# Optimization experiments

Hardware: AMD Instinct MI355X
Metric: run time of the kernel (lower is better)

The kernel has to match this reference:

```python
import jax, jax.numpy as jnp
import numpy as np

N_NODES = 100000
N_EDGES = 800000
IN_CH = 100
HID = 100   # 2 * out_channels
OUT = 50


def setup_inputs() -> dict:
    key = jax.random.key(0)
    ks = jax.random.split(key, 6)
    x = jax.random.normal(ks[0], (N_NODES, IN_CH), dtype=jnp.float32)
    edge_index = jax.random.randint(ks[1], (2, N_EDGES), 0, N_NODES, dtype=jnp.int32)
    # Glorot-ish init for the three GCN layer weights; zero biases.
    W1 = jax.random.normal(ks[2], (IN_CH, HID), dtype=jnp.float32) * (1.0 / np.sqrt(IN_CH))
    b1 = jnp.zeros((HID,), dtype=jnp.float32)
    W_mu = jax.random.normal(ks[3], (HID, OUT), dtype=jnp.float32) * (1.0 / np.sqrt(HID))
    b_mu = jnp.zeros((OUT,), dtype=jnp.float32)
    W_ls = jax.random.normal(ks[4], (HID, OUT), dtype=jnp.float32) * (1.0 / np.sqrt(HID))
    b_ls = jnp.zeros((OUT,), dtype=jnp.float32)
    return {"x": x, "edge_index": edge_index, "W1": W1, "b1": b1,
            "W_mu": W_mu, "b_mu": b_mu, "W_ls": W_ls, "b_ls": b_ls}


def _gcn_conv(x, W, b, src, dst, deg_inv_sqrt, n):
    # GCNConv: out = D^-1/2 (A + I) D^-1/2 (x W) + b
    h = x @ W                                      # transform first (smaller messages)
    norm = deg_inv_sqrt[src] * deg_inv_sqrt[dst]   # [E]
    agg = jax.ops.segment_sum(h[src] * norm[:, None], dst, num_segments=n)
    agg = agg + h * (deg_inv_sqrt * deg_inv_sqrt)[:, None]  # self-loop term
    return agg + b


def reference(x, edge_index, W1, b1, W_mu, b_mu, W_ls, b_ls):
    n = x.shape[0]
    src, dst = edge_index[0], edge_index[1]
    # degree with self-loops (GCN normalization, edge_weight = 1)
    deg = jax.ops.segment_sum(jnp.ones((edge_index.shape[1],), jnp.float32), dst,
                              num_segments=n) + 1.0
    deg_inv_sqrt = jax.lax.rsqrt(deg)
    h = jax.nn.relu(_gcn_conv(x, W1, b1, src, dst, deg_inv_sqrt, n))
    # dropout is identity in eval mode (p applied only during training)
    mu = _gcn_conv(h, W_mu, b_mu, src, dst, deg_inv_sqrt, n)
    logstd = _gcn_conv(h, W_ls, b_ls, src, dst, deg_inv_sqrt, n)
    return mu, logstd
```

## Files before the change

kernel.cpp:

```cpp
#include <hip/hip_runtime.h>

#define NN 100000
#define NE 800000
#define NBLK 196
#define BCAP 6144
#define EPB 8192
#define NPART ((NE + EPB - 1) / EPB)
#define PACKBLK 56
#define HS 112

typedef unsigned short ushort_t;
typedef unsigned int uint_t;
typedef __attribute__((ext_vector_type(8))) short short8;
typedef __attribute__((ext_vector_type(4))) float floatx4;

__device__ __forceinline__ float bf2f(ushort_t u) {
    union { unsigned int i; float f; } v; v.i = ((unsigned int)u) << 16; return v.f;
}
__device__ __forceinline__ ushort_t f2bf(float f) {
    union { float f; unsigned int i; } v; v.f = f;
    unsigned int b = v.i + 0x7FFF + ((v.i >> 16) & 1);
    return (ushort_t)(b >> 16);
}
__device__ __forceinline__ uint_t pack2(float a, float b) {
    return (uint_t)f2bf(a) | ((uint_t)f2bf(b) << 16);
}

__global__ __launch_bounds__(256) void k_part(const int* __restrict__ src,
                                              const int* __restrict__ dst,
                                              int* __restrict__ bcnt,
                                              int* __restrict__ bedge,
                                              const float* __restrict__ W1,
                                              const float* __restrict__ Wmu,
                                              const float* __restrict__ Wls,
                                              uint_t* __restrict__ Wt1g,
                                              uint_t* __restrict__ Wt2g) {
    __shared__ int hist[NBLK];
    __shared__ int lbase[NBLK];
    const int blk = blockIdx.x, t = threadIdx.x;

    if (blk >= NPART) {
        int lidx = (blk - NPART) * 256 + t;
        int np = lidx >> 6;
        int kp = lidx & 63;
        int mat = np / 112, n = np - mat * 112;
        int k0 = kp * 2, k1 = k0 + 1;
        float w0 = 0.0f, w1 = 0.0f;
        if (mat == 0) {
            if (n < 100) {
                if (k0 < 100) w0 = W1[k0 * 100 + n];
                if (k1 < 100) w1 = W1[k1 * 100 + n];
            }
            Wt1g[n * 64 + kp] = pack2(w0, w1);
        } else {
            if (n < 50) {
                if (k0 < 100) w0 = Wmu[k0 * 50 + n];
                if (k1 < 100) w1 = Wmu[k1 * 50 + n];
            } else if (n < 100) {
                if (k0 < 100) w0 = Wls[k0 * 50 + (n - 50)];
                if (k1 < 100) w1 = Wls[k1 * 50 + (n - 50)];
            }
            Wt2g[n * 64 + kp] = pack2(w0, w1);
        }
        return;
    }

    const int e0 = blk * EPB;
    const int e1 = (e0 + EPB < NE) ? e0 + EPB : NE;

    if (t < NBLK) hist[t] = 0;
    __syncthreads();
    for (int e = e0 + t; e < e1; e += 256)
        atomicAdd(&hist[dst[e] >> 9], 1);
    __syncthreads();
    if (t < NBLK) {
        int h = hist[t];
        lbase[t] = (h > 0) ? atomicAdd(&bcnt[t], h) : 0;
    }
    __syncthreads();
    if (t < NBLK) hist[t] = lbase[t];
    __syncthreads();
    for (int e = e0 + t; e < e1; e += 256) {
        int d = dst[e];
        int b = d >> 9;
        int pos = atomicAdd(&hist[b], 1);
        bedge[b * BCAP + pos] = src[e] | ((d & 511) << 17);
    }
}

__global__ __launch_bounds__(256) void k_build(const int* __restrict__ bcnt,
                                               const int* __restrict__ bedge,
                                               float* __restrict__ dis,
                                               int* __restrict__ off,
                                               int* __restrict__ ssrc) {
    __shared__ int eb[BCAP];
    __shared__ int hist[512];
    __shared__ int sc[2][512];
    __shared__ int red[4];
    const int b = blockIdx.x, t = threadIdx.x;
    const int cnt = bcnt[b];
    const int* be = bedge + (size_t)b * BCAP;
    const int g0 = b * 512;

    hist[t] = 0; hist[t + 256] = 0;
    int part = (t < b) ? bcnt[t] : 0;
    #pragma unroll
    for (int o = 32; o > 0; o >>= 1) part += __shfl_down(part, o, 64);
    if ((t & 63) == 0) red[t >> 6] = part;
    __syncthreads();

    for (int i = t; i < cnt; i += 256) {
        int v = be[i];
        eb[i] = v;
        atomicAdd(&hist[v >> 17], 1);
    }
    __syncthreads();
    const int base0 = red[0] + red[1] + red[2] + red[3];

    sc[0][t] = hist[t];
    sc[0][t + 256] = hist[t + 256];
    __syncthreads();
    int c = 0;
    for (int o = 1; o < 512; o <<= 1) {
        int nxt = c ^ 1;
        #pragma unroll
        for (int q = 0; q < 2; ++q) {
            int j = t + q * 256;
            sc[nxt][j] = sc[c][j] + ((j >= o) ? sc[c][j - o] : 0);
        }
        c = nxt;
        __syncthreads();
    }

    #pragma unroll
    for (int q = 0; q < 2; ++q) {
        int j = t + q * 256, g = g0 + j;
        int o = base0 + ((j > 0) ? sc[c][j - 1] : 0);
        if (g < NN) dis[g] = rsqrtf((float)hist[j] + 1.0f);
        if (g <= NN) off[g] = o;
        hist[j] = o;
    }
    __syncthreads();

    for (int i = t; i < cnt; i += 256) {
        int v = eb[i];
        int pos = atomicAdd(&hist[v >> 17], 1);
        ssrc[pos] = v & 0x1FFFF;
    }
}

__global__ __launch_bounds__(256) void k_gemm1_mfma(
    const float* __restrict__ X, const uint_t* __restrict__ Wtg,
    const float* __restrict__ dis,
    ushort_t* __restrict__ H)
{
    __shared__ ushort_t Ws[112 * 136];
    const int tid = threadIdx.x;
    const int row0 = blockIdx.x * 64;

    for (int idx = tid; idx < 112 * 16; idx += 256) {
        int n = idx >> 4, c = idx & 15;
        uint4 v = *(const uint4*)&Wtg[n * 64 + c * 4];
        *(uint4*)&Ws[n * 136 + c * 8] = v;
    }
    __syncthreads();

    const int wave = tid >> 6, lane = tid & 63;
    const int quad = lane >> 4, l16 = lane & 15;
    int row = row0 + wave * 16 + l16;
    if (row >= NN) row = NN - 1;
    const float* xp = X + (size_t)row * 100;

    floatx4 acc[7];
    #pragma unroll
    for (int t = 0; t < 7; ++t) acc[t] = (floatx4){0.f, 0.f, 0.f, 0.f};

    #pragma unroll
    for (int ks = 0; ks < 4; ++ks) {
        const int kb = ks * 32 + quad * 8;
        short8 af;
        if (ks < 3) {
            float4 u = *(const float4*)&xp[kb];
            float4 v = *(const float4*)&xp[kb + 4];
            af[0] = (short)f2bf(u.x); af[1] = (short)f2bf(u.y);
            af[2] = (short)f2bf(u.z); af[3] = (short)f2bf(u.w);
            af[4] = (short)f2bf(v.x); af[5] = (short)f2bf(v.y);
            af[6] = (short)f2bf(v.z); af[7] = (short)f2bf(v.w);
        } else {
            af = (short8){0, 0, 0, 0, 0, 0, 0, 0};
            if (quad == 0) {
                float4 u = *(const float4*)&xp[96];
                af[0] = (short)f2bf(u.x); af[1] = (short)f2bf(u.y);
                af[2] = (short)f2bf(u.z); af[3] = (short)f2bf(u.w);
            }
        }
        #pragma unroll
        for (int t = 0; t < 7; ++t) {
            short8 bf = *(const short8*)&Ws[(t * 16 + l16) * 136 + kb];
            acc[t] = __builtin_amdgcn_mfma_f32_16x16x32_bf16(af, bf, acc[t], 0, 0, 0);
        }
    }

    const int mbase = row0 + wave * 16 + quad * 4;
    #pragma unroll
    for (int reg = 0; reg < 4; ++reg) {
        int m = mbase + reg;
        if (m >= NN) continue;
        float dd = dis[m];
        #pragma unroll
        for (int t = 0; t < 7; ++t) {
            int n = t * 16 + l16;
            H[(size_t)m * HS + n] = (n < 100) ? f2bf(acc[t][reg] * dd) : (ushort_t)0;
        }
    }
}

__global__ __launch_bounds__(256) void k_gemm2_mfma(
    const ushort_t* __restrict__ A,
    const uint_t* __restrict__ Wtg,
    const float* __restrict__ bmu, const float* __restrict__ bls,
    float* __restrict__ outmu, float* __restrict__ outls)
{
    __shared__ ushort_t Ws[112 * 136];
    const int tid = threadIdx.x;
    const int row0 = blockIdx.x * 64;

    for (int idx = tid; idx < 112 * 16; idx += 256) {
        int n = idx >> 4, c = idx & 15;
        uint4 v = *(const uint4*)&Wtg[n * 64 + c * 4];
        *(uint4*)&Ws[n * 136 + c * 8] = v;
    }
    __syncthreads();

    const int wave = tid >> 6, lane = tid & 63;
    const int quad = lane >> 4, l16 = lane & 15;
    int arow = row0 + wave * 16 + l16;
    if (arow >= NN) arow = NN - 1;
    const ushort_t* ap = A + (size_t)arow * HS;

    floatx4 acc[7];
    #pragma unroll
    for (int t = 0; t < 7; ++t) acc[t] = (floatx4){0.f, 0.f, 0.f, 0.f};

    #pragma unroll
    for (int ks = 0; ks < 4; ++ks) {
        const int k0 = ks * 32;
        short8 af;
        if (ks < 3) {
            af = *(const short8*)&ap[k0 + quad * 8];
        } else {
            if (quad < 2) af = *(const short8*)&ap[96 + quad * 8];
            else af = (short8){0, 0, 0, 0, 0, 0, 0, 0};
        }
        #pragma unroll
        for (int t = 0; t < 7; ++t) {
            short8 bf = *(const short8*)&Ws[(t * 16 + l16) * 136 + k0 + quad * 8];
            acc[t] = __builtin_amdgcn_mfma_f32_16x16x32_bf16(af, bf, acc[t], 0, 0, 0);
        }
    }

    const int mbase = row0 + wave * 16 + quad * 4;
    #pragma unroll
    for (int reg = 0; reg < 4; ++reg) {
        int m = mbase + reg;
        if (m >= NN) continue;
        #pragma unroll
        for (int t = 0; t < 7; ++t) {
            int n = t * 16 + l16;
            if (n < 50) {
                outmu[(size_t)m * 50 + n] = acc[t][reg] + bmu[n];
            } else if (n < 100) {
                outls[(size_t)m * 50 + (n - 50)] = acc[t][reg] + bls[n - 50];
            }
        }
    }
}

template<int PHASE>
__global__ __launch_bounds__(256, 4) void k_agg(
    const ushort_t* __restrict__ Hin,
    const int* __restrict__ off, const int* __restrict__ ssrc,
    const float* __restrict__ dis, const float* __restrict__ bias,
    ushort_t* __restrict__ outb)
{
    int i = blockIdx.x * 256 + threadIdx.x;
    if (i >= NN * 7) return;
    int node = i / 7;
    int col = (i - node * 7) * 16;
    const ushort_t* hbase = Hin + col;

    float d = dis[node];
    float a[16];
    {
        short8 u = *(const short8*)(hbase + (size_t)node * HS);
        short8 v = *(const short8*)(hbase + (size_t)node * HS + 8);
        #pragma unroll
        for (int j = 0; j < 8; ++j) { a[j] = bf2f((ushort_t)u[j]); a[8 + j] = bf2f((ushort_t)v[j]); }
    }

    int e0 = off[node], e1 = off[node + 1];
    int e = e0;
    for (; e + 7 < e1; e += 8) {
        int s[8];
        #pragma unroll
        for (int q = 0; q < 8; ++q) s[q] = ssrc[e + q];
        short8 uu[8], vv[8];
        #pragma unroll
        for (int q = 0; q < 8; ++q) {
            uu[q] = *(const short8*)(hbase + (size_t)s[q] * HS);
            vv[q] = *(const short8*)(hbase + (size_t)s[q] * HS + 8);
        }
        #pragma unroll
        for (int q = 0; q < 8; ++q) {
            #pragma unroll
            for (int j = 0; j < 8; ++j) {
                a[j]     += bf2f((ushort_t)uu[q][j]);
                a[8 + j] += bf2f((ushort_t)vv[q][j]);
            }
        }
    }
    for (; e + 3 < e1; e += 4) {
        int s[4];
        #pragma unroll
        for (int q = 0; q < 4; ++q) s[q] = ssrc[e + q];
        short8 uu[4], vv[4];
        #pragma unroll
        for (int q = 0; q < 4; ++q) {
            uu[q] = *(const short8*)(hbase + (size_t)s[q] * HS);
            vv[q] = *(const short8*)(hbase + (size_t)s[q] * HS + 8);
        }
        #pragma unroll
        for (int q = 0; q < 4; ++q) {
            #pragma unroll
            for (int j = 0; j < 8; ++j) {
                a[j]     += bf2f((ushort_t)uu[q][j]);
                a[8 + j] += bf2f((ushort_t)vv[q][j]);
            }
        }
    }
    for (; e < e1; ++e) {
        int s0 = ssrc[e];
        short8 u0 = *(const short8*)(hbase + (size_t)s0 * HS);
        short8 v0 = *(const short8*)(hbase + (size_t)s0 * HS + 8);
        #pragma unroll
        for (int j = 0; j < 8; ++j) {
            a[j] += bf2f((ushort_t)u0[j]);
            a[8 + j] += bf2f((ushort_t)v0[j]);
        }
    }

    short8 o0, o1;
    if (PHASE == 1) {
        float b[16];
        #pragma unroll
        for (int j = 0; j < 16; ++j) {
            int cj = col + j;
            b[j] = (cj < 100) ? bias[cj] : 0.0f;
        }
        #pragma unroll
        for (int j = 0; j < 8; ++j) {
            float h0 = fmaxf(a[j] * d + b[j], 0.0f) * d;
            float h1 = fmaxf(a[8 + j] * d + b[8 + j], 0.0f) * d;
            o0[j] = (short)f2bf(h0);
            o1[j] = (short)f2bf(h1);
        }
    } else {
        #pragma unroll
        for (int j = 0; j < 8; ++j) {
            o0[j] = (short)f2bf(a[j] * d);
            o1[j] = (short)f2bf(a[8 + j] * d);
        }
    }
    *(short8*)(outb + (size_t)node * HS + col) = o0;
    *(short8*)(outb + (size_t)node * HS + col + 8) = o1;
}

extern "C" void kernel_launch(void* const* d_in, const int* in_sizes, int n_in,
                              void* d_out, int out_size, void* d_ws, size_t ws_size,
                              hipStream_t stream)
{
    const float* x   = (const float*)d_in[0];
    const int*   ei  = (const int*)d_in[1];
    const float* W1  = (const float*)d_in[2];
    const float* b1  = (const float*)d_in[3];
    const float* Wmu = (const float*)d_in[4];
    const float* bmu = (const float*)d_in[5];
    const float* Wls = (const float*)d_in[6];
    const float* bls = (const float*)d_in[7];
    float* out = (float*)d_out;

    const int* src = ei;
    const int* dst = ei + NE;

    int*   wsI  = (int*)d_ws;
    float* wsF  = (float*)d_ws;
    int*      off  = wsI + 100000;
    float*    dis  = wsF + 200704;
    uint_t*   Wt1g = (uint_t*)(wsI + 300704);
    uint_t*   Wt2g = (uint_t*)(wsI + 307872);
    int*      bcnt = wsI + 315040;
    int*      ssrc = wsI + 315296;
    int*      bedge= wsI + 1115296;
    ushort_t* H1b  = (ushort_t*)(wsI + 2319520);
    ushort_t* hb   = (ushort_t*)(wsI + 8719520);
    ushort_t* A2b  = (ushort_t*)(wsI + 15119520);
    (void)ws_size;

    hipMemsetAsync(bcnt, 0, 256 * sizeof(int), stream);
    k_part<<<NPART + PACKBLK, 256, 0, stream>>>(src, dst, bcnt, bedge,
                                                W1, Wmu, Wls, Wt1g, Wt2g);
    k_build<<<NBLK, 256, 0, stream>>>(bcnt, bedge, dis, off, ssrc);

    const int gblk = (NN + 63) / 64;
    const int ablk = (NN * 7 + 255) / 256;
    k_gemm1_mfma<<<gblk, 256, 0, stream>>>(x, Wt1g, dis, H1b);
    k_agg<1><<<ablk, 256, 0, stream>>>(H1b, off, ssrc, dis, b1, hb);
    k_agg<2><<<ablk, 256, 0, stream>>>(hb, off, ssrc, dis, b1, A2b);
    k_gemm2_mfma<<<gblk, 256, 0, stream>>>(A2b, Wt2g, bmu, bls,
                                           out, out + (size_t)NN * 50);
}
```

Before: 249.9 us.

## Store hidden features in column-slice-major layout and loop slices per node in aggregation

Hidden features are now stored as seven column slices of 16 bf16 values, each slice laid out contiguously across all nodes, instead of 112-wide rows. The aggregation kernel assigns two threads per node, which split that node's edges and loop over the seven slices in turn, combining their partial sums with a lane shuffle. The intent is to shrink the gather working set per pass so each slice (about 3.2 MB) stays in cache, improving reuse of random neighbor reads. In exchange there are far fewer threads (2 per node instead of 7), each doing a serial loop over slices, and the edge indices are re-read once per slice.

```diff
diff --git a/kernel.cpp b/kernel.cpp
--- a/kernel.cpp
+++ b/kernel.cpp
@@ -7,7 +7,8 @@
 #define EPB 8192
 #define NPART ((NE + EPB - 1) / EPB)
 #define PACKBLK 56
-#define HS 112
+#define NSL 7
+#define SLSZ ((size_t)NN * 16)
 
 typedef unsigned short ushort_t;
 typedef unsigned int uint_t;
@@ -210,7 +211,8 @@
         #pragma unroll
         for (int t = 0; t < 7; ++t) {
             int n = t * 16 + l16;
-            H[(size_t)m * HS + n] = (n < 100) ? f2bf(acc[t][reg] * dd) : (ushort_t)0;
+            H[(size_t)t * SLSZ + (size_t)m * 16 + l16] =
+                (n < 100) ? f2bf(acc[t][reg] * dd) : (ushort_t)0;
         }
     }
 }
@@ -236,7 +238,6 @@
     const int quad = lane >> 4, l16 = lane & 15;
     int arow = row0 + wave * 16 + l16;
     if (arow >= NN) arow = NN - 1;
-    const ushort_t* ap = A + (size_t)arow * HS;
 
     floatx4 acc[7];
     #pragma unroll
@@ -244,17 +245,17 @@
 
     #pragma unroll
     for (int ks = 0; ks < 4; ++ks) {
-        const int k0 = ks * 32;
+        const int c0 = ks * 32 + quad * 8;
+        const int g = c0 >> 4, woff = c0 & 8;
         short8 af;
-        if (ks < 3) {
-            af = *(const short8*)&ap[k0 + quad * 8];
+        if (g < 7) {
+            af = *(const short8*)&A[(size_t)g * SLSZ + (size_t)arow * 16 + woff];
         } else {
-            if (quad < 2) af = *(const short8*)&ap[96 + quad * 8];
-            else af = (short8){0, 0, 0, 0, 0, 0, 0, 0};
+            af = (short8){0, 0, 0, 0, 0, 0, 0, 0};
         }
         #pragma unroll
         for (int t = 0; t < 7; ++t) {
-            short8 bf = *(const short8*)&Ws[(t * 16 + l16) * 136 + k0 + quad * 8];
+            short8 bf = *(const short8*)&Ws[(t * 16 + l16) * 136 + ks * 32 + quad * 8];
             acc[t] = __builtin_amdgcn_mfma_f32_16x16x32_bf16(af, bf, acc[t], 0, 0, 0);
         }
     }
@@ -277,102 +278,107 @@
 }
 
 template<int PHASE>
-__global__ __launch_bounds__(256, 4) void k_agg(
+__global__ __launch_bounds__(256) void k_agg(
     const ushort_t* __restrict__ Hin,
     const int* __restrict__ off, const int* __restrict__ ssrc,
     const float* __restrict__ dis, const float* __restrict__ bias,
     ushort_t* __restrict__ outb)
 {
     int i = blockIdx.x * 256 + threadIdx.x;
-    if (i >= NN * 7) return;
-    int node = i / 7;
-    int col = (i - node * 7) * 16;
-    const ushort_t* hbase = Hin + col;
-
+    int node = i >> 1, rep = i & 1;
+    if (node >= NN) return;
     float d = dis[node];
-    float a[16];
-    {
-        short8 u = *(const short8*)(hbase + (size_t)node * HS);
-        short8 v = *(const short8*)(hbase + (size_t)node * HS + 8);
-        #pragma unroll
-        for (int j = 0; j < 8; ++j) { a[j] = bf2f((ushort_t)u[j]); a[8 + j] = bf2f((ushort_t)v[j]); }
-    }
-
     int e0 = off[node], e1 = off[node + 1];
-    int e = e0;
-    for (; e + 7 < e1; e += 8) {
-        int s[8];
-        #pragma unroll
-        for (int q = 0; q < 8; ++q) s[q] = ssrc[e + q];
-        short8 uu[8], vv[8];
-        #pragma unroll
-        for (int q = 0; q < 8; ++q) {
-            uu[q] = *(const short8*)(hbase + (size_t)s[q] * HS);
-            vv[q] = *(const short8*)(hbase + (size_t)s[q] * HS + 8);
-        }
-        #pragma unroll
-        for (int q = 0; q < 8; ++q) {
+
+    #pragma unroll 1
+    for (int s = 0; s < NSL; ++s) {
+        const ushort_t* hb = Hin + (size_t)s * SLSZ;
+        float a[16];
+        if (rep == 0) {
+            short8 u = *(const short8*)(hb + (size_t)node * 16);
+            short8 v = *(const short8*)(hb + (size_t)node * 16 + 8);
+            #pragma unroll
+            for (int j = 0; j < 8; ++j) { a[j] = bf2f((ushort_t)u[j]); a[8 + j] = bf2f((ushort_t)v[j]); }
+        } else {
+            #pragma unroll
+            for (int j = 0; j < 16; ++j) a[j] = 0.0f;
+        }
+
+        int e = e0 + rep;
+        for (; e + 14 < e1; e += 16) {
+            int sq[8];
+            #pragma unroll
+            for (int q = 0; q < 8; ++q) sq[q] = ssrc[e + 2 * q];
+            short8 uu[8], vv[8];
+            #pragma unroll
+            for (int q = 0; q < 8; ++q) {
+                uu[q] = *(const short8*)(hb + (size_t)sq[q] * 16);
+                vv[q] = *(const short8*)(hb + (size_t)sq[q] * 16 + 8);
+            }
+            #pragma unroll
+            for (int q = 0; q < 8; ++q) {
+                #pragma unroll
+                for (int j = 0; j < 8; ++j) {
+                    a[j]     += bf2f((ushort_t)uu[q][j]);
+                    a[8 + j] += bf2f((ushort_t)vv[q][j]);
+                }
+            }
+        }
+        for (; e + 6 < e1; e += 8) {
+            int sq[4];
+            #pragma unroll
+            for (int q = 0; q < 4; ++q) sq[q] = ssrc[e + 2 * q];
+            short8 uu[4], vv[4];
+            #pragma unroll
+            for (int q = 0; q < 4; ++q) {
+                uu[q] = *(const short8*)(hb + (size_t)sq[q] * 16);
+                vv[q] = *(const short8*)(hb + (size_t)sq[q] * 16 + 8);
+            }
+            #pragma unroll
+            for (int q = 0; q < 4; ++q) {
+                #pragma unroll
+                for (int j = 0; j < 8; ++j) {
+                    a[j]     += bf2f((ushort_t)uu[q][j]);
+                    a[8 + j] += bf2f((ushort_t)vv[q][j]);
+                }
+            }
+        }
+        for (; e < e1; e += 2) {
+            int s0 = ssrc[e];
+            short8 u0 = *(const short8*)(hb + (size_t)s0 * 16);
+            short8 v0 = *(const short8*)(hb + (size_t)s0 * 16 + 8);
             #pragma unroll
             for (int j = 0; j < 8; ++j) {
-                a[j]     += bf2f((ushort_t)uu[q][j]);
-                a[8 + j] += bf2f((ushort_t)vv[q][j]);
-            }
-        }
-    }
-    for (; e + 3 < e1; e += 4) {
-        int s[4];
-        #pragma unroll
-        for (int q = 0; q < 4; ++q) s[q] = ssrc[e + q];
-        short8 uu[4], vv[4];
-        #pragma unroll
-        for (int q = 0; q < 4; ++q) {
-            uu[q] = *(const short8*)(hbase + (size_t)s[q] * HS);
-            vv[q] = *(const short8*)(hbase + (size_t)s[q] * HS + 8);
-        }
-        #pragma unroll
-        for (int q = 0; q < 4; ++q) {
-            #pragma unroll
-            for (int j = 0; j < 8; ++j) {
-                a[j]     += bf2f((ushort_t)uu[q][j]);
-                a[8 + j] += bf2f((ushort_t)vv[q][j]);
-            }
-        }
-    }
-    for (; e < e1; ++e) {
-        int s0 = ssrc[e];
-        short8 u0 = *(const short8*)(hbase + (size_t)s0 * HS);
-        short8 v0 = *(const short8*)(hbase + (size_t)s0 * HS + 8);
-        #pragma unroll
-        for (int j = 0; j < 8; ++j) {
-            a[j] += bf2f((ushort_t)u0[j]);
-            a[8 + j] += bf2f((ushort_t)v0[j]);
-        }
-    }
-
-    short8 o0, o1;
-    if (PHASE == 1) {
-        float b[16];
-        #pragma unroll
-        for (int j = 0; j < 16; ++j) {
-            int cj = col + j;
-            b[j] = (cj < 100) ? bias[cj] : 0.0f;
-        }
-        #pragma unroll
-        for (int j = 0; j < 8; ++j) {
-            float h0 = fmaxf(a[j] * d + b[j], 0.0f) * d;
-            float h1 = fmaxf(a[8 + j] * d + b[8 + j], 0.0f) * d;
-            o0[j] = (short)f2bf(h0);
-            o1[j] = (short)f2bf(h1);
-        }
-    } else {
-        #pragma unroll
-        for (int j = 0; j < 8; ++j) {
-            o0[j] = (short)f2bf(a[j] * d);
-            o1[j] = (short)f2bf(a[8 + j] * d);
-        }
-    }
-    *(short8*)(outb + (size_t)node * HS + col) = o0;
-    *(short8*)(outb + (size_t)node * HS + col + 8) = o1;
+                a[j] += bf2f((ushort_t)u0[j]);
+                a[8 + j] += bf2f((ushort_t)v0[j]);
+            }
+        }
+
+        #pragma unroll
+        for (int j = 0; j < 16; ++j) a[j] += __shfl_xor(a[j], 1, 64);
+
+        if (rep == 0) {
+            short8 o0, o1;
+            if (PHASE == 1) {
+                #pragma unroll
+                for (int j = 0; j < 8; ++j) {
+                    int c0 = s * 16 + j, c1 = s * 16 + 8 + j;
+                    float b0 = (c0 < 100) ? bias[c0] : 0.0f;
+                    float b1v = (c1 < 100) ? bias[c1] : 0.0f;
+                    o0[j] = (short)f2bf(fmaxf(a[j] * d + b0, 0.0f) * d);
+                    o1[j] = (short)f2bf(fmaxf(a[8 + j] * d + b1v, 0.0f) * d);
+                }
+            } else {
+                #pragma unroll
+                for (int j = 0; j < 8; ++j) {
+                    o0[j] = (short)f2bf(a[j] * d);
+                    o1[j] = (short)f2bf(a[8 + j] * d);
+                }
+            }
+            *(short8*)(outb + (size_t)s * SLSZ + (size_t)node * 16) = o0;
+            *(short8*)(outb + (size_t)s * SLSZ + (size_t)node * 16 + 8) = o1;
+        }
+    }
 }
 
 extern "C" void kernel_launch(void* const* d_in, const int* in_sizes, int n_in,
@@ -412,7 +418,7 @@
     k_build<<<NBLK, 256, 0, stream>>>(bcnt, bedge, dis, off, ssrc);
 
     const int gblk = (NN + 63) / 64;
-    const int ablk = (NN * 7 + 255) / 256;
+    const int ablk = (2 * NN + 255) / 256;
     k_gemm1_mfma<<<gblk, 256, 0, stream>>>(x, Wt1g, dis, H1b);
     k_agg<1><<<ablk, 256, 0, stream>>>(H1b, off, ssrc, dis, b1, hb);
     k_agg<2><<<ablk, 256, 0, stream>>>(hb, off, ssrc, dis, b1, A2b);
```

Result: slower. 329.8 us (+31.9%).

## Pad feature rows to 128 and split each node's edges across two lanes

Applied to the files above, without the earlier changes.

The bf16 feature row stride grows from 112 to 128 elements, so every row starts on a 256-byte boundary. The aggregation kernel now gives each node 16 lanes: 8 column chunks times 2 edge-parity halves. The two halves are summed with a lane shuffle, and only the even lane writes the result. The goal is more memory-level parallelism and aligned gathers in the latency-bound neighbour gather, at the cost of an extra all-zero column chunk and more threads launched. The second GEMM's K loop simplifies because the padding columns are now explicitly zero.

```diff
diff --git a/kernel.cpp b/kernel.cpp
--- a/kernel.cpp
+++ b/kernel.cpp
@@ -7,7 +7,6 @@
 #define EPB 8192
 #define NPART ((NE + EPB - 1) / EPB)
 #define PACKBLK 56
-#define HS 112
 
 typedef unsigned short ushort_t;
 typedef unsigned int uint_t;
@@ -210,8 +209,9 @@
         #pragma unroll
         for (int t = 0; t < 7; ++t) {
             int n = t * 16 + l16;
-            H[(size_t)m * HS + n] = (n < 100) ? f2bf(acc[t][reg] * dd) : (ushort_t)0;
-        }
+            H[(size_t)m * 128 + n] = (n < 100) ? f2bf(acc[t][reg] * dd) : (ushort_t)0;
+        }
+        H[(size_t)m * 128 + 112 + l16] = 0;
     }
 }
 
@@ -236,22 +236,14 @@
     const int quad = lane >> 4, l16 = lane & 15;
     int arow = row0 + wave * 16 + l16;
     if (arow >= NN) arow = NN - 1;
-    const ushort_t* ap = A + (size_t)arow * HS;
 
     floatx4 acc[7];
     #pragma unroll
     for (int t = 0; t < 7; ++t) acc[t] = (floatx4){0.f, 0.f, 0.f, 0.f};
 
     #pragma unroll
-    for (int ks = 0; ks < 4; ++ks) {
-        const int k0 = ks * 32;
-        short8 af;
-        if (ks < 3) {
-            af = *(const short8*)&ap[k0 + quad * 8];
-        } else {
-            if (quad < 2) af = *(const short8*)&ap[96 + quad * 8];
-            else af = (short8){0, 0, 0, 0, 0, 0, 0, 0};
-        }
+    for (int k0 = 0; k0 < 128; k0 += 32) {
+        short8 af = *(const short8*)&A[(size_t)arow * 128 + k0 + quad * 8];
         #pragma unroll
         for (int t = 0; t < 7; ++t) {
             short8 bf = *(const short8*)&Ws[(t * 16 + l16) * 136 + k0 + quad * 8];
@@ -284,31 +276,36 @@
     ushort_t* __restrict__ outb)
 {
     int i = blockIdx.x * 256 + threadIdx.x;
-    if (i >= NN * 7) return;
-    int node = i / 7;
-    int col = (i - node * 7) * 16;
+    if (i >= NN * 16) return;
+    int node = i >> 4;
+    int sub = i & 15;
+    int rep = sub & 1;
+    int col = (sub >> 1) * 16;
     const ushort_t* hbase = Hin + col;
 
     float d = dis[node];
     float a[16];
-    {
-        short8 u = *(const short8*)(hbase + (size_t)node * HS);
-        short8 v = *(const short8*)(hbase + (size_t)node * HS + 8);
+    if (rep == 0) {
+        short8 u = *(const short8*)(hbase + (size_t)node * 128);
+        short8 v = *(const short8*)(hbase + (size_t)node * 128 + 8);
         #pragma unroll
         for (int j = 0; j < 8; ++j) { a[j] = bf2f((ushort_t)u[j]); a[8 + j] = bf2f((ushort_t)v[j]); }
+    } else {
+        #pragma unroll
+        for (int j = 0; j < 16; ++j) a[j] = 0.0f;
     }
 
     int e0 = off[node], e1 = off[node + 1];
-    int e = e0;
-    for (; e + 7 < e1; e += 8) {
+    int e = e0 + rep;
+    for (; e + 14 < e1; e += 16) {
         int s[8];
         #pragma unroll
-        for (int q = 0; q < 8; ++q) s[q] = ssrc[e + q];
+        for (int q = 0; q < 8; ++q) s[q] = ssrc[e + 2 * q];
         short8 uu[8], vv[8];
         #pragma unroll
         for (int q = 0; q < 8; ++q) {
-            uu[q] = *(const short8*)(hbase + (size_t)s[q] * HS);
-            vv[q] = *(const short8*)(hbase + (size_t)s[q] * HS + 8);
+            uu[q] = *(const short8*)(hbase + (size_t)s[q] * 128);
+            vv[q] = *(const short8*)(hbase + (size_t)s[q] * 128 + 8);
         }
         #pragma unroll
         for (int q = 0; q < 8; ++q) {
@@ -319,15 +316,15 @@
             }
         }
     }
-    for (; e + 3 < e1; e += 4) {
+    for (; e + 6 < e1; e += 8) {
         int s[4];
         #pragma unroll
-        for (int q = 0; q < 4; ++q) s[q] = ssrc[e + q];
+        for (int q = 0; q < 4; ++q) s[q] = ssrc[e + 2 * q];
         short8 uu[4], vv[4];
         #pragma unroll
         for (int q = 0; q < 4; ++q) {
-            uu[q] = *(const short8*)(hbase + (size_t)s[q] * HS);
-            vv[q] = *(const short8*)(hbase + (size_t)s[q] * HS + 8);
+            uu[q] = *(const short8*)(hbase + (size_t)s[q] * 128);
+            vv[q] = *(const short8*)(hbase + (size_t)s[q] * 128 + 8);
         }
         #pragma unroll
         for (int q = 0; q < 4; ++q) {
@@ -338,10 +335,10 @@
             }
         }
     }
-    for (; e < e1; ++e) {
+    for (; e < e1; e += 2) {
         int s0 = ssrc[e];
-        short8 u0 = *(const short8*)(hbase + (size_t)s0 * HS);
-        short8 v0 = *(const short8*)(hbase + (size_t)s0 * HS + 8);
+        short8 u0 = *(const short8*)(hbase + (size_t)s0 * 128);
+        short8 v0 = *(const short8*)(hbase + (size_t)s0 * 128 + 8);
         #pragma unroll
         for (int j = 0; j < 8; ++j) {
             a[j] += bf2f((ushort_t)u0[j]);
@@ -349,30 +346,35 @@
         }
     }
 
-    short8 o0, o1;
-    if (PHASE == 1) {
-        float b[16];
-        #pragma unroll
-        for (int j = 0; j < 16; ++j) {
-            int cj = col + j;
-            b[j] = (cj < 100) ? bias[cj] : 0.0f;
-        }
-        #pragma unroll
-        for (int j = 0; j < 8; ++j) {
-            float h0 = fmaxf(a[j] * d + b[j], 0.0f) * d;
-            float h1 = fmaxf(a[8 + j] * d + b[8 + j], 0.0f) * d;
-            o0[j] = (short)f2bf(h0);
-            o1[j] = (short)f2bf(h1);
-        }
-    } else {
-        #pragma unroll
-        for (int j = 0; j < 8; ++j) {
-            o0[j] = (short)f2bf(a[j] * d);
-            o1[j] = (short)f2bf(a[8 + j] * d);
-        }
-    }
-    *(short8*)(outb + (size_t)node * HS + col) = o0;
-    *(short8*)(outb + (size_t)node * HS + col + 8) = o1;
+    #pragma unroll
+    for (int j = 0; j < 16; ++j) a[j] += __shfl_xor(a[j], 1, 64);
+
+    if (rep == 0) {
+        short8 o0, o1;
+        if (PHASE == 1) {
+            float b[16];
+            #pragma unroll
+            for (int j = 0; j < 16; ++j) {
+                int cj = col + j;
+                b[j] = (cj < 100) ? bias[cj] : 0.0f;
+            }
+            #pragma unroll
+            for (int j = 0; j < 8; ++j) {
+                float h0 = fmaxf(a[j] * d + b[j], 0.0f) * d;
+                float h1 = fmaxf(a[8 + j] * d + b[8 + j], 0.0f) * d;
+                o0[j] = (short)f2bf(h0);
+                o1[j] = (short)f2bf(h1);
+            }
+        } else {
+            #pragma unroll
+            for (int j = 0; j < 8; ++j) {
+                o0[j] = (short)f2bf(a[j] * d);
+                o1[j] = (short)f2bf(a[8 + j] * d);
+            }
+        }
+        *(short8*)(outb + (size_t)node * 128 + col) = o0;
+        *(short8*)(outb + (size_t)node * 128 + col + 8) = o1;
+    }
 }
 
 extern "C" void kernel_launch(void* const* d_in, const int* in_sizes, int n_in,
@@ -412,7 +414,7 @@
     k_build<<<NBLK, 256, 0, stream>>>(bcnt, bedge, dis, off, ssrc);
 
     const int gblk = (NN + 63) / 64;
-    const int ablk = (NN * 7 + 255) / 256;
+    const int ablk = (NN * 16 + 255) / 256;
     k_gemm1_mfma<<<gblk, 256, 0, stream>>>(x, Wt1g, dis, H1b);
     k_agg<1><<<ablk, 256, 0, stream>>>(H1b, off, ssrc, dis, b1, hb);
     k_agg<2><<<ablk, 256, 0, stream>>>(hb, off, ssrc, dis, b1, A2b);
```

Result: slower. 269.2 us (+7.7%).
